# Kernel tuning notes

Hardware: AMD Instinct MI355X
Metric: run time of the kernel (lower is better)

## Reference

```python
import jax, jax.numpy as jnp
import numpy as np

N, E, F_DIM = 30000, 480000, 256
CLS_HID, NUM_CLASS, GEN_HID, MI_HID, BATCH = 128, 16, 64, 128, 4096
COM_L1, COM_L2, LAM, ALPHA, TAU, EPS = 0.5, 0.5, 0.5, 1.0, 0.5, 1e-8


def _glorot(key, shape):
    scale = jnp.sqrt(2.0 / (shape[0] + shape[-1]))
    return scale * jax.random.normal(key, shape, dtype=jnp.float32)


def setup_inputs() -> dict:
    key = jax.random.key(0)
    ks = jax.random.split(key, 32)
    inp = {
        'feat': jax.random.normal(ks[0], (N, F_DIM), dtype=jnp.float32),
        'view1_indices': jax.random.randint(ks[1], (2, E), 0, N),
        'view1_values': jax.random.uniform(ks[2], (E,), dtype=jnp.float32),
        'view2_indices': jax.random.randint(ks[3], (2, E), 0, N),
        'view2_values': jax.random.uniform(ks[4], (E,), dtype=jnp.float32),
        'idx': jnp.sort(jax.random.randint(ks[5], (BATCH,), 0, N)),
        # GenView (v1 and v2): gen_gcn weight + gen_mlp (Linear(2*gen_hid, 1))
        'W_gen_v1': _glorot(ks[6], (F_DIM, GEN_HID)),
        'Wm_v1': _glorot(ks[7], (2 * GEN_HID, 1)),
        'bm_v1': jnp.zeros((1,), dtype=jnp.float32),
        'W_gen_v2': _glorot(ks[8], (F_DIM, GEN_HID)),
        'Wm_v2': _glorot(ks[9], (2 * GEN_HID, 1)),
        'bm_v2': jnp.zeros((1,), dtype=jnp.float32),
        # Classification: three two-layer GCN encoders (v1, v2, v)
        'W1_v1': _glorot(ks[10], (F_DIM, CLS_HID)), 'W2_v1': _glorot(ks[11], (CLS_HID, NUM_CLASS)),
        'W1_v2': _glorot(ks[12], (F_DIM, CLS_HID)), 'W2_v2': _glorot(ks[13], (CLS_HID, NUM_CLASS)),
        'W1_v': _glorot(ks[14], (F_DIM, CLS_HID)), 'W2_v': _glorot(ks[15], (CLS_HID, NUM_CLASS)),
        # MI_NCE: three single GCN layers + shared projection MLP
        'Wg': _glorot(ks[16], (F_DIM, MI_HID)),
        'Wg1': _glorot(ks[17], (F_DIM, MI_HID)),
        'Wg2': _glorot(ks[18], (F_DIM, MI_HID)),
        'Wp1': _glorot(ks[19], (MI_HID, MI_HID)), 'bp1': jnp.zeros((MI_HID,), dtype=jnp.float32),
        'Wp2': _glorot(ks[20], (MI_HID, MI_HID)), 'bp2': jnp.zeros((MI_HID,), dtype=jnp.float32),
    }
    return inp


def spmm(idx, vals, x, n):
    # sparse COO adj (idx [2,E], vals [E]) @ dense x [n,d]
    return jax.ops.segment_sum(vals[:, None] * x[idx[1]], idx[0], num_segments=n)


def gcn_layer(x, idx, vals, W, n, act):
    h = spmm(idx, vals, x @ W, n)
    return jax.nn.relu(h) if act else h


def two_layer(x, idx, vals, W1, W2, n):
    return gcn_layer(gcn_layer(x, idx, vals, W1, n, True), idx, vals, W2, n, False)


def sparse_row_softmax(scores, rows, n):
    m = jax.lax.stop_gradient(jax.ops.segment_max(scores, rows, num_segments=n))
    e = jnp.exp(scores - m[rows])
    s = jax.ops.segment_sum(e, rows, num_segments=n)
    return e / s[rows]


def gen_view(feat, idx, vals, Wg, Wm, bm, com_lambda, n):
    emb = gcn_layer(feat, idx, vals, Wg, n, True)
    ff = jnp.concatenate([emb[idx[0]], emb[idx[1]]], axis=-1)  # [E, 2*gen_hid]
    temp = (ff @ Wm + bm).reshape(-1)
    pi = sparse_row_softmax(temp, idx[0], n)  # torch.sparse.softmax(dim=1)
    return vals + com_lambda * pi  # same sparsity pattern as v_ori


def sym(idx, vals):
    # normalize1 (big=True): adj + adj.T as COO concat (duplicates sum in spmm)
    return jnp.concatenate([idx, idx[::-1]], axis=1), jnp.concatenate([vals, vals])


def get_weight(prob):
    top2 = jax.lax.top_k(prob, 2)[0]
    fir, sec = top2[:, 0], top2[:, 1]
    return jnp.exp(ALPHA * (LAM * jnp.log(fir + EPS) + (1.0 - LAM) * jnp.log(fir - sec + EPS)))


def contrast_cal(z1, z2):
    num = z1 @ z2.T
    den = jnp.linalg.norm(z1, axis=-1, keepdims=True) @ jnp.linalg.norm(z2, axis=-1, keepdims=True).T
    m12 = jnp.exp(num / den / TAU)
    m21 = m12.T
    l12 = -jnp.log(jnp.diag(m12 / (m12.sum(1, keepdims=True) + EPS)) + EPS).mean()
    l21 = -jnp.log(jnp.diag(m21 / (m21.sum(1, keepdims=True) + EPS)) + EPS).mean()
    return 0.5 * (l12 + l21)


def cogsl_forward(feat, view1_values, view2_values,
                  W_gen_v1, Wm_v1, bm_v1, W_gen_v2, Wm_v2, bm_v2,
                  W1_v1, W2_v1, W1_v2, W2_v2, W1_v, W2_v,
                  Wg, Wg1, Wg2, Wp1, bp1, Wp2, bp2,
                  view1_indices, view2_indices, idx):
    n = feat.shape[0]
    # View_Estimator (GenView + normalize1)
    nv1 = gen_view(feat, view1_indices, view1_values, W_gen_v1, Wm_v1, bm_v1, COM_L1, n)
    nv2 = gen_view(feat, view2_indices, view2_values, W_gen_v2, Wm_v2, bm_v2, COM_L2, n)
    i1, v1 = sym(view1_indices, nv1)
    i2, v2 = sym(view2_indices, nv2)
    # Classification on each generated view
    prob_v1 = jax.nn.softmax(two_layer(feat, i1, v1, W1_v1, W2_v1, n), axis=1)
    prob_v2 = jax.nn.softmax(two_layer(feat, i2, v2, W1_v2, W2_v2, n), axis=1)
    logits_v1 = jnp.log(prob_v1 + EPS)
    logits_v2 = jnp.log(prob_v2 + EPS)
    # Fusion: per-node convex combination of the two sparse views (row scaling)
    w1 = get_weight(prob_v1)
    w2 = get_weight(prob_v2)
    b1 = w1 / (w1 + w2)
    b2 = w2 / (w1 + w2)
    idx_f = jnp.concatenate([i1, i2], axis=1)
    vals_f = jnp.concatenate([b1[i1[0]] * v1, b2[i2[0]] * v2])
    prob_v = jax.nn.softmax(two_layer(feat, idx_f, vals_f, W1_v, W2_v, n), axis=1)
    logits_v = jnp.log(prob_v + EPS)
    # MI_NCE over [fused v, v1, v2], big=True -> sample `batch` nodes
    proj = lambda h: jax.nn.elu(h @ Wp1 + bp1) @ Wp2 + bp2
    ev = proj(gcn_layer(feat, idx_f, vals_f, Wg, n, True))[idx]
    e1 = proj(gcn_layer(feat, i1, v1, Wg1, n, True))[idx]
    e2 = proj(gcn_layer(feat, i2, v2, Wg2, n, True))[idx]
    vv1 = contrast_cal(ev, e1)
    vv2 = contrast_cal(ev, e2)
    v1v2 = contrast_cal(e1, e2)
    return jnp.concatenate([logits_v.ravel(), logits_v1.ravel(), logits_v2.ravel(),
                            jnp.stack([vv1, vv2, v1v2])])


def reference(feat, view1_indices, view1_values, view2_indices, view2_values, idx,
              W_gen_v1, Wm_v1, bm_v1, W_gen_v2, Wm_v2, bm_v2,
              W1_v1, W2_v1, W1_v2, W2_v2, W1_v, W2_v,
              Wg, Wg1, Wg2, Wp1, bp1, Wp2, bp2):
    return cogsl_forward(feat, view1_values, view2_values,
                         W_gen_v1, Wm_v1, bm_v1, W_gen_v2, Wm_v2, bm_v2,
                         W1_v1, W2_v1, W1_v2, W2_v2, W1_v, W2_v,
                         Wg, Wg1, Wg2, Wp1, bp1, Wp2, bp2,
                         view1_indices, view2_indices, idx)
```

## Files before the change

### kernel.cpp

```cpp
#include <hip/hip_runtime.h>
#include <math.h>

#define NN 30000
#define EE 480000
#define FD 256
#define CH 128
#define NCLS 16
#define GH 64
#define MH 128
#define BT 4096
#define EPSc 1e-8f
#define GBc ((NN + 127) / 128)
#define SPB8 ((NN + 7) / 8)
#define SPB16 ((NN + 15) / 16)
#define RBc ((BT + 15) / 16)
#define PRB ((NN + 63) / 64)
#define PJB (BT / 8)
#define PX4 1056

typedef __attribute__((ext_vector_type(8))) short short8;
typedef __attribute__((ext_vector_type(4))) float f32x4;

__device__ __forceinline__ unsigned short f2bf(float x) {
    unsigned b = __float_as_uint(x);
    unsigned r = b + 0x7FFFu + ((b >> 16) & 1u);
    return (unsigned short)(r >> 16);
}
__device__ __forceinline__ float bf2f(unsigned short h) {
    return __uint_as_float(((unsigned)h) << 16);
}
__device__ __forceinline__ float4 fma4(float s, float4 x, float4 a) {
    a.x = fmaf(s, x.x, a.x); a.y = fmaf(s, x.y, a.y);
    a.z = fmaf(s, x.z, a.z); a.w = fmaf(s, x.w, a.w);
    return a;
}

struct WSArgs {
    const float* s[8];
    unsigned short* h[8];
    unsigned short* l[8];
};

__global__ __launch_bounds__(256) void prep_all(
    const float* __restrict__ feat, unsigned short* __restrict__ fhi,
    unsigned short* __restrict__ flo, WSArgs a,
    const int* __restrict__ i1, const int* __restrict__ i2, int* __restrict__ cnt,
    int* __restrict__ sd1, int* __restrict__ sd2,
    int* __restrict__ sc1, int* __restrict__ sc2)
{
    int b = blockIdx.x;
    if (b < 30000) {
        long i = (long)b * 256 + threadIdx.x;
        float v = feat[i];
        unsigned short h = f2bf(v);
        fhi[i] = h;
        flo[i] = f2bf(v - bf2f(h));
        return;
    }
    b -= 30000;
    if (b < 896) {
        int i = b * 256 + threadIdx.x;
        if (i >= 229376) return;
        constexpr int NNp[8] = {64, 64, 128, 128, 128, 128, 128, 128};
        constexpr int OFF[9] = {0, 16384, 32768, 65536, 98304, 131072, 163840, 196608, 229376};
        int w = 0;
#pragma unroll
        for (int t = 1; t < 8; t++) if (i >= OFF[t]) w = t;
        int j = i - OFF[w];
        int N = NNp[w];
        int k = j / N, n = j % N;
        float v = a.s[w][j];
        unsigned short hh = f2bf(v);
        a.h[w][(size_t)n * 256 + k] = hh;
        a.l[w][(size_t)n * 256 + k] = f2bf(v - bf2f(hh));
        return;
    }
    b -= 896;
    int e = b * 256 + threadIdx.x;
    if (e >= EE) return;
    int r1 = i1[e], c1 = i1[EE + e];
    int r2 = i2[e], c2 = i2[EE + e];
    sd1[e] = atomicAdd(&cnt[r1], 1);
    sd2[e] = atomicAdd(&cnt[NN + r2], 1);
    sc1[e] = atomicAdd(&cnt[2 * NN + c1], 1);
    sc2[e] = atomicAdd(&cnt[3 * NN + c2], 1);
}

template <int NT, bool OUT16>
__device__ __forceinline__ void gemm3_body(
    unsigned short* sm, int bx,
    const unsigned short* __restrict__ Ahi, const unsigned short* __restrict__ Alo,
    const unsigned short* __restrict__ BThi, const unsigned short* __restrict__ BTlo,
    int K, void* __restrict__ Cv, int Cstride, int M)
{
    unsigned short* Ah = sm;
    unsigned short* Al = Ah + 128 * 40;
    unsigned short* Bh = Al + 128 * 40;
    unsigned short* Bl = Bh + NT * 16 * 40;
    int t = threadIdx.x;
    int w = t >> 6, l = t & 63;
    int lane = l & 15, quad = l >> 4;
// ... 65 lines not shown
            for (int n = 0; n < NT; n++) {
                if (OUT16)
                    ((unsigned short*)Cv)[(size_t)gr * Cstride + n * 16 + lane] = f2bf(acc[s][n][reg]);
                else
                    ((float*)Cv)[(size_t)gr * Cstride + n * 16 + lane] = acc[s][n][reg];
            }
        }
    }
}

template <int NT, bool OUT16>
__device__ __forceinline__ void gemm1_body(
    unsigned short* sm, int bx,
    const unsigned short* __restrict__ Ahi,
    const unsigned short* __restrict__ BThi,
    int K, void* __restrict__ Cv, int Cstride, int M)
{
    unsigned short* Ah = sm;
    unsigned short* Bh = Ah + 128 * 40;
    int t = threadIdx.x;
    int w = t >> 6, l = t & 63;
    int lane = l & 15, quad = l >> 4;
    int row0 = bx * 128;
    f32x4 acc[2][NT];
#pragma unroll
    for (int s = 0; s < 2; s++)
#pragma unroll
        for (int n = 0; n < NT; n++) acc[s][n] = (f32x4)(0.f);

    int ar = t >> 1, ako = (t & 1) << 4;
    int nkc = K >> 5;
    for (int kc = 0; kc < nkc; kc++) {
        int kb = kc << 5;
        {
            int gr = row0 + ar;
            float4 h0, h1;
            if (gr < M) {
                const float4* pH = (const float4*)&Ahi[(size_t)gr * K + kb + ako];
                h0 = pH[0]; h1 = pH[1];
            } else {
                h0 = h1 = make_float4(0.f, 0.f, 0.f, 0.f);
            }
            float4* dH = (float4*)&Ah[ar * 40 + ako];
            dH[0] = h0; dH[1] = h1;
        }
        if (ar < NT * 16) {
            const float4* pH = (const float4*)&BThi[(size_t)ar * K + kb + ako];
            float4 h0 = pH[0], h1 = pH[1];
            float4* dH = (float4*)&Bh[ar * 40 + ako];
            dH[0] = h0; dH[1] = h1;
        }
        __syncthreads();
        short8 aH[2];
#pragma unroll
        for (int s = 0; s < 2; s++)
            aH[s] = *(const short8*)&Ah[(w * 32 + s * 16 + lane) * 40 + quad * 8];
#pragma unroll
        for (int n = 0; n < NT; n++) {
            short8 bH = *(const short8*)&Bh[(n * 16 + lane) * 40 + quad * 8];
#pragma unroll
            for (int s = 0; s < 2; s++)
                acc[s][n] = __builtin_amdgcn_mfma_f32_16x16x32_bf16(aH[s], bH, acc[s][n], 0, 0, 0);
        }
        __syncthreads();
    }
#pragma unroll
    for (int s = 0; s < 2; s++) {
        int rb = row0 + w * 32 + s * 16 + quad * 4;
#pragma unroll
        for (int reg = 0; reg < 4; reg++) {
            int gr = rb + reg;
            if (gr >= M) continue;
#pragma unroll
            for (int n = 0; n < NT; n++) {
                if (OUT16)
                    ((unsigned short*)Cv)[(size_t)gr * Cstride + n * 16 + lane] = f2bf(acc[s][n][reg]);
                else
                    ((float*)Cv)[(size_t)gr * Cstride + n * 16 + lane] = acc[s][n][reg];
            }
        }
    }
}

__global__ __launch_bounds__(256) void mega1x(
    const int* __restrict__ i1, const float* __restrict__ v1,
    const int* __restrict__ i2, const float* __restrict__ v2,
    const int* __restrict__ sd1, const int* __restrict__ sd2,
    const int* __restrict__ sc1, const int* __restrict__ sc2,
    const int* __restrict__ rp4,
    int2* __restrict__ ed1, int2* __restrict__ ec1,
    int2* __restrict__ ed2, int2* __restrict__ ec2,
    const unsigned short* __restrict__ feat_hi, const unsigned short* __restrict__ feat_lo,
    const unsigned short* __restrict__ wgen12h, const unsigned short* __restrict__ wgen12l,
    float* __restrict__ Pg,
    const unsigned short* __restrict__ w1pairh, const unsigned short* __restrict__ w1pairl,
    float* __restrict__ P01,
    const unsigned short* __restrict__ w1vh, unsigned short* __restrict__ Ph2,
    const unsigned short* __restrict__ wgallh, unsigned short* __restrict__ Pmi16)
{
    __shared__ unsigned short sm[128 * 40 * 2 + 8 * 16 * 40 * 2];
    int b = blockIdx.x;
    if (b < GBc) {
        gemm3_body<8, false>(sm, b, feat_hi, feat_lo, wgen12h, wgen12l, FD, Pg, 128, NN);
        return;
    }
    b -= GBc;
    if (b < 2 * GBc) {
        int y = b / GBc, bx = b % GBc;
        gemm3_body<8, false>(sm, bx, feat_hi, feat_lo,
                             w1pairh + (size_t)y * 32768, w1pairl + (size_t)y * 32768,
                             FD, P01 + (size_t)y * 128, 256, NN);
        return;
    }
    b -= 2 * GBc;
    if (b < GBc) {
        gemm1_body<8, true>(sm, b, feat_hi, w1vh, FD, Ph2, 128, NN);
        return;
    }
    b -= GBc;
    if (b < 3 * GBc) {
        int y = b / GBc, bx = b % GBc;
        gemm1_body<8, true>(sm, bx, feat_hi, wgallh + (size_t)y * 32768,
                            FD, Pmi16 + (size_t)y * 128, 384, NN);
        return;
    }
    b -= 3 * GBc;
    int e = b * 256 + threadIdx.x;
    if (e >= EE) return;
    const int* rp_d1 = rp4;
    const int* rp_d2 = rp4 + (NN + 1);
    const int* rp_c1 = rp4 + 2 * (NN + 1);
    const int* rp_c2 = rp4 + 3 * (NN + 1);
    int r = i1[e], c = i1[EE + e];
    int p = rp_d1[r] + sd1[e];
    ed1[p] = make_int2(c, __float_as_int(v1[e]));
    ec1[rp_c1[c] + sc1[e]] = make_int2(r, p);
    r = i2[e]; c = i2[EE + e];
    p = rp_d2[r] + sd2[e];
    ed2[p] = make_int2(c, __float_as_int(v2[e]));
    ec2[rp_c2[c] + sc2[e]] = make_int2(r, p);
}

__global__ __launch_bounds__(256) void contrast_direct(
    const unsigned short* __restrict__ z16, float* __restrict__ stats)
{
    int p = blockIdx.z;
    int pa = (p == 2) ? 1 : 0;
    int pb = (p == 0) ? 1 : 2;
    const unsigned short* A = z16 + (size_t)pa * BT * MH;
    const unsigned short* B = z16 + (size_t)pb * BT * MH;
    float* diag = stats + (size_t)p * 3 * BT;
    float* rs = diag + BT;
    float* cs = rs + BT;
    int t = threadIdx.x;
    int w = t >> 6, l = t & 63, m = l & 15, quad = l >> 4;
    int i0 = blockIdx.y * 128, j0 = blockIdx.x * 128;

    short8 afr[2][4];
#pragma unroll
    for (int s = 0; s < 2; s++) {
        const unsigned short* arow = &A[(size_t)(i0 + w * 32 + s * 16 + m) * MH + quad * 8];
#pragma unroll
        for (int kc = 0; kc < 4; kc++)
            afr[s][kc] = *(const short8*)(arow + kc * 32);
    }
    f32x4 acc[2][8];
#pragma unroll
    for (int s = 0; s < 2; s++)
#pragma unroll
        for (int n = 0; n < 8; n++) acc[s][n] = (f32x4)(0.f);

#pragma unroll
    for (int kc = 0; kc < 4; kc++) {
#pragma unroll
        for (int n = 0; n < 8; n++) {
            short8 bf = *(const short8*)&B[(size_t)(j0 + n * 16 + m) * MH + kc * 32 + quad * 8];
            acc[0][n] = __builtin_amdgcn_mfma_f32_16x16x32_bf16(afr[0][kc], bf, acc[0][n], 0, 0, 0);
            acc[1][n] = __builtin_amdgcn_mfma_f32_16x16x32_bf16(afr[1][kc], bf, acc[1][n], 0, 0, 0);
        }
    }
    float colp[8];
#pragma unroll
    for (int n = 0; n < 8; n++) colp[n] = 0.f;
#pragma unroll
    for (int s = 0; s < 2; s++) {
        int rbase = i0 + w * 32 + s * 16 + quad * 4;
#pragma unroll
        for (int reg = 0; reg < 4; reg++) {
            float rsum = 0.f;
            int gi = rbase + reg;
#pragma unroll
            for (int n = 0; n < 8; n++) {
                float mv = expf(acc[s][n][reg] * 2.0f);
                rsum += mv;
                colp[n] += mv;
                int gj = j0 + n * 16 + m;
                if (gi == gj) diag[gi] = mv;
            }
            rsum += __shfl_xor(rsum, 1); rsum += __shfl_xor(rsum, 2);
            rsum += __shfl_xor(rsum, 4); rsum += __shfl_xor(rsum, 8);
            if (m == 0) atomicAdd(&rs[gi], rsum);
        }
    }
    __shared__ float scol[128];
    if (t < 128) scol[t] = 0.f;
    __syncthreads();
#pragma unroll
    for (int n = 0; n < 8; n++) {
        float v = colp[n];
        v += __shfl_xor(v, 16); v += __shfl_xor(v, 32);
        if (quad == (n & 3)) atomicAdd(&scol[n * 16 + m], v);
    }
    __syncthreads();
    if (t < 128) atomicAdd(&cs[j0 + t], scol[t]);
}

__global__ __launch_bounds__(1024) void scan_block4(const int* __restrict__ cnt,
                                                    int* __restrict__ rowptr,
                                                    int* __restrict__ bsum) {
    int y = blockIdx.y;
    int* rp = rowptr + y * (NN + 1);
    int* bs = bsum + y * 32;
    __shared__ int tmp[1024];
    int t = threadIdx.x;
    int i = blockIdx.x * 1024 + t;
    int v = (i < NN) ? cnt[y * NN + i] : 0;
    tmp[t] = v;
    __syncthreads();
    for (int off = 1; off < 1024; off <<= 1) {
        int add = (t >= off) ? tmp[t - off] : 0;
        __syncthreads();
        tmp[t] += add;
        __syncthreads();
    }
    if (i <= NN) rp[i] = tmp[t] - v;
    if (t == 1023) bs[blockIdx.x] = tmp[1023];
}
__global__ void scan_bsum4(int* __restrict__ bsum, int nb) {
    bsum += blockIdx.x * 32;
    int t = threadIdx.x;
    int orig = (t < nb) ? bsum[t] : 0;
    int v = orig;
    for (int off = 1; off < 64; off <<= 1) {
        int u = __shfl_up(v, off);
        if (t >= off) v += u;
    }
    if (t < nb) bsum[t] = v - orig;
}
__global__ void scan_add4(const int* __restrict__ bsum, int* __restrict__ rowptr) {
    int y = blockIdx.y;
    const int* bs = bsum + y * 32;
    int* rp = rowptr + y * (NN + 1);
    int i = blockIdx.x * 1024 + threadIdx.x;
    if (i <= NN) rp[i] += bs[blockIdx.x];
}

__global__ __launch_bounds__(256) void gen_nv(
    const int* __restrict__ rp_d, int2* __restrict__ ed1, int2* __restrict__ ed2,
    const float* __restrict__ sb, float* __restrict__ nvd1, float* __restrict__ nvd2)
{
    int y = blockIdx.y;
    int row = blockIdx.x * 256 + threadIdx.x;
    if (row >= NN) return;
    const int* rp = rp_d + y * (NN + 1);
    int2* ed = y ? ed2 : ed1;
    float* nvd = y ? nvd2 : nvd1;
    const float* sbv = sb + (size_t)y * NN;
    int p0 = rp[row], p1 = rp[row + 1];
    float m = -3.4e38f, sum = 0.f;
    for (int j = p0; j < p1; j++) {
        float x = sbv[ed[j].x];
        if (x > m) { sum = sum * expf(m - x) + 1.f; m = x; }
        else sum += expf(x - m);
    }
    float inv = 1.f / sum;
    for (int j = p0; j < p1; j++) {
        int2 q = ed[j];
        float nv = __int_as_float(q.y) + 0.5f * expf(sbv[q.x] - m) * inv;
        nvd[j] = nv;
        ed[j].y = __float_as_int(nv);
    }
}

template <int STR4>
__device__ __forceinline__ void gath_dir_f32(
    const int* __restrict__ rp, const int2* __restrict__ ed, int row,
    const float4* __restrict__ x4, int xo, float4* a)
{
    int p0 = rp[row], p1 = rp[row + 1];
    int j = p0;
    for (; j + 8 <= p1; j += 8) {
        int2 q0 = ed[j], q1 = ed[j+1], q2 = ed[j+2], q3 = ed[j+3];
        int2 q4 = ed[j+4], q5 = ed[j+5], q6 = ed[j+6], q7 = ed[j+7];
        float4 x0 = x4[(size_t)q0.x * STR4 + xo];
        float4 x1 = x4[(size_t)q1.x * STR4 + xo];
        float4 x2 = x4[(size_t)q2.x * STR4 + xo];
        float4 x3 = x4[(size_t)q3.x * STR4 + xo];
        float4 x5 = x4[(size_t)q4.x * STR4 + xo];
        float4 x6 = x4[(size_t)q5.x * STR4 + xo];
        float4 x7 = x4[(size_t)q6.x * STR4 + xo];
        float4 x8 = x4[(size_t)q7.x * STR4 + xo];
        a[0] = fma4(__int_as_float(q0.y), x0, a[0]);
        a[1] = fma4(__int_as_float(q1.y), x1, a[1]);
        a[2] = fma4(__int_as_float(q2.y), x2, a[2]);
        a[3] = fma4(__int_as_float(q3.y), x3, a[3]);
        a[0] = fma4(__int_as_float(q4.y), x5, a[0]);
        a[1] = fma4(__int_as_float(q5.y), x6, a[1]);
        a[2] = fma4(__int_as_float(q6.y), x7, a[2]);
        a[3] = fma4(__int_as_float(q7.y), x8, a[3]);
    }
    for (; j + 4 <= p1; j += 4) {
        int2 q0 = ed[j], q1 = ed[j+1], q2 = ed[j+2], q3 = ed[j+3];
        a[0] = fma4(__int_as_float(q0.y), x4[(size_t)q0.x * STR4 + xo], a[0]);
        a[1] = fma4(__int_as_float(q1.y), x4[(size_t)q1.x * STR4 + xo], a[1]);
        a[2] = fma4(__int_as_float(q2.y), x4[(size_t)q2.x * STR4 + xo], a[2]);
        a[3] = fma4(__int_as_float(q3.y), x4[(size_t)q3.x * STR4 + xo], a[3]);
    }
    for (; j < p1; j++) {
        int2 q = ed[j];
        a[0] = fma4(__int_as_float(q.y), x4[(size_t)q.x * STR4 + xo], a[0]);
    }
}
template <int STR4>
__device__ __forceinline__ void gath_csc_f32(
    const int* __restrict__ rp, const int2* __restrict__ ec, const float* __restrict__ nvd,
    int row, const float4* __restrict__ x4, int xo, float4* a)
{
    int p0 = rp[row], p1 = rp[row + 1];
    int j = p0;
    for (; j + 8 <= p1; j += 8) {
        int2 q0 = ec[j], q1 = ec[j+1], q2 = ec[j+2], q3 = ec[j+3];
        int2 q4 = ec[j+4], q5 = ec[j+5], q6 = ec[j+6], q7 = ec[j+7];
        float4 x0 = x4[(size_t)q0.x * STR4 + xo];
        float4 x1 = x4[(size_t)q1.x * STR4 + xo];
        float4 x2 = x4[(size_t)q2.x * STR4 + xo];
        float4 x3 = x4[(size_t)q3.x * STR4 + xo];
        float4 x5 = x4[(size_t)q4.x * STR4 + xo];
        float4 x6 = x4[(size_t)q5.x * STR4 + xo];
        float4 x7 = x4[(size_t)q6.x * STR4 + xo];
        float4 x8 = x4[(size_t)q7.x * STR4 + xo];
        float v0 = nvd[q0.y], v1 = nvd[q1.y], v2 = nvd[q2.y], v3 = nvd[q3.y];
        float v4 = nvd[q4.y], v5 = nvd[q5.y], v6 = nvd[q6.y], v7 = nvd[q7.y];
        a[0] = fma4(v0, x0, a[0]);
        a[1] = fma4(v1, x1, a[1]);
        a[2] = fma4(v2, x2, a[2]);
        a[3] = fma4(v3, x3, a[3]);
        a[0] = fma4(v4, x5, a[0]);
        a[1] = fma4(v5, x6, a[1]);
        a[2] = fma4(v6, x7, a[2]);
        a[3] = fma4(v7, x8, a[3]);
    }
    for (; j + 4 <= p1; j += 4) {
        int2 q0 = ec[j], q1 = ec[j+1], q2 = ec[j+2], q3 = ec[j+3];
        float v0 = nvd[q0.y], v1 = nvd[q1.y], v2 = nvd[q2.y], v3 = nvd[q3.y];
        a[0] = fma4(v0, x4[(size_t)q0.x * STR4 + xo], a[0]);
        a[1] = fma4(v1, x4[(size_t)q1.x * STR4 + xo], a[1]);
        a[2] = fma4(v2, x4[(size_t)q2.x * STR4 + xo], a[2]);
        a[3] = fma4(v3, x4[(size_t)q3.x * STR4 + xo], a[3]);
    }
    for (; j < p1; j++) {
        int2 q = ec[j];
        a[0] = fma4(nvd[q.y], x4[(size_t)q.x * STR4 + xo], a[0]);
    }
}

__global__ __launch_bounds__(256) void spmm64_scores(
    const int* __restrict__ rp_d, const int2* __restrict__ e1, const int2* __restrict__ e2,
    const float* __restrict__ Pg, const float* __restrict__ Wm1,
    const float* __restrict__ Wm2, float* __restrict__ sb)
{
    int y = blockIdx.y;
    const int* rp = rp_d + y * (NN + 1);
    const int2* arr = y ? e2 : e1;
    int row = blockIdx.x * 16 + threadIdx.x / 16;
    int o = threadIdx.x % 16;
    if (row >= NN) return;
    float4 a[4] = {};
    gath_dir_f32<32>(rp, arr, row, (const float4*)Pg, y * 16 + o, a);
    float4 r;
    r.x = fmaxf((a[0].x + a[1].x) + (a[2].x + a[3].x), 0.f);
    r.y = fmaxf((a[0].y + a[1].y) + (a[2].y + a[3].y), 0.f);
    r.z = fmaxf((a[0].z + a[1].z) + (a[2].z + a[3].z), 0.f);
    r.w = fmaxf((a[0].w + a[1].w) + (a[2].w + a[3].w), 0.f);
    const float* Wmh = (y ? Wm2 : Wm1) + GH;
    float part = r.x * Wmh[o * 4] + r.y * Wmh[o * 4 + 1]
               + r.z * Wmh[o * 4 + 2] + r.w * Wmh[o * 4 + 3];
    part += __shfl_xor(part, 1); part += __shfl_xor(part, 2);
    part += __shfl_xor(part, 4); part += __shfl_xor(part, 8);
    if (o == 0) sb[y * NN + row] = part;
}

__device__ __forceinline__ void softmax16_epi(
    float4 r, int node, float* __restrict__ logits, float* __restrict__ wout)
{
    int o = threadIdx.x & 3;
    float mx = fmaxf(fmaxf(r.x, r.y), fmaxf(r.z, r.w));
    mx = fmaxf(mx, __shfl_xor(mx, 1));
    mx = fmaxf(mx, __shfl_xor(mx, 2));
    float e0 = expf(r.x - mx), e1 = expf(r.y - mx), e2 = expf(r.z - mx), e3 = expf(r.w - mx);
    float s = (e0 + e1) + (e2 + e3);
    s += __shfl_xor(s, 1);
    s += __shfl_xor(s, 2);
    float inv = 1.f / s;
    float p0 = e0 * inv, p1 = e1 * inv, p2 = e2 * inv, p3 = e3 * inv;
    float4 lg;
    lg.x = logf(p0 + EPSc); lg.y = logf(p1 + EPSc);
    lg.z = logf(p2 + EPSc); lg.w = logf(p3 + EPSc);
    ((float4*)logits)[(size_t)node * 4 + o] = lg;
    if (wout) {
        float f = p0, se = -1.f;
        if (p1 > f) { se = f; f = p1; } else se = p1;
        if (p2 > f) { se = f; f = p2; } else if (p2 > se) se = p2;
        if (p3 > f) { se = f; f = p3; } else if (p3 > se) se = p3;
#pragma unroll
        for (int d = 1; d <= 2; d <<= 1) {
            float of = __shfl_xor(f, d), os = __shfl_xor(se, d);
            if (of > f) { se = fmaxf(f, os); f = of; }
            else se = fmaxf(se, of);
        }
        if (o == 0)
            wout[node] = expf(0.5f * logf(f + EPSc) + 0.5f * logf(f - se + EPSc));
    }
}

__device__ __forceinline__ void pair_body(
    int y, int bx, const int* __restrict__ rp_d, const int* __restrict__ rp_c,
    const int2* __restrict__ ed1, const int2* __restrict__ ec1, const float* __restrict__ nvd1,
    const int2* __restrict__ ed2, const int2* __restrict__ ec2, const float* __restrict__ nvd2,
    const float* __restrict__ R01, float* __restrict__ logits_base, float* __restrict__ w12)
{
    const int* rpd = rp_d + y * (NN + 1);
    const int* rpc = rp_c + y * (NN + 1);
    const int2* ed = y ? ed2 : ed1;
    const int2* ec = y ? ec2 : ec1;
    const float* nvd = y ? nvd2 : nvd1;
    int row = bx * 64 + threadIdx.x / 4;
    int o = threadIdx.x % 4;
    if (row >= NN) return;
    const float4* x4 = (const float4*)(R01 + (size_t)y * NN * 16);
    float4 a[4] = {};
    gath_dir_f32<4>(rpd, ed, row, x4, o, a);
    gath_csc_f32<4>(rpc, ec, nvd, row, x4, o, a);
    float4 r;
    r.x = (a[0].x + a[1].x) + (a[2].x + a[3].x);
    r.y = (a[0].y + a[1].y) + (a[2].y + a[3].y);
    r.z = (a[0].z + a[1].z) + (a[2].z + a[3].z);
    r.w = (a[0].w + a[1].w) + (a[2].w + a[3].w);
    softmax16_epi(r, row, logits_base + (size_t)y * NN * NCLS, w12 + (size_t)y * NN);
}

__device__ __forceinline__ void fused_body(
    int bx, const int* __restrict__ rp_d, const int* __restrict__ rp_c,
    const int2* __restrict__ ed1, const int2* __restrict__ ec1, const float* __restrict__ nvd1,
    const int2* __restrict__ ed2, const int2* __restrict__ ec2, const float* __restrict__ nvd2,
    const float* __restrict__ w12, const float* __restrict__ x, float* __restrict__ logits)
{
    int row = bx * 64 + threadIdx.x / 4;
    int o = threadIdx.x % 4;
    if (row >= NN) return;
    const float4* x4 = (const float4*)x;
    float4 a[4] = {};
    gath_dir_f32<4>(rp_d, ed1, row, x4, o, a);
    gath_csc_f32<4>(rp_c, ec1, nvd1, row, x4, o, a);
    float4 s1;
    s1.x = (a[0].x + a[1].x) + (a[2].x + a[3].x);
    s1.y = (a[0].y + a[1].y) + (a[2].y + a[3].y);
    s1.z = (a[0].z + a[1].z) + (a[2].z + a[3].z);
    s1.w = (a[0].w + a[1].w) + (a[2].w + a[3].w);
    float4 b[4] = {};
    gath_dir_f32<4>(rp_d + (NN + 1), ed2, row, x4, o, b);
    gath_csc_f32<4>(rp_c + (NN + 1), ec2, nvd2, row, x4, o, b);
    float4 s2;
// ... 220 lines not shown

__global__ __launch_bounds__(256) void mega2(
    const int* __restrict__ rp_d, const int* __restrict__ rp_c,
    const int2* __restrict__ ed1, const int2* __restrict__ ec1, const float* __restrict__ nvd1,
    const int2* __restrict__ ed2, const int2* __restrict__ ec2, const float* __restrict__ nvd2,
    const float* __restrict__ P01, const float* __restrict__ W2v1, const float* __restrict__ W2v2,
    float* __restrict__ R01,
    const int* __restrict__ rows, const unsigned short* __restrict__ Pmi,
    float* __restrict__ zQ)
{
    __shared__ float sm[2048 + 8 * 128];
    int b = blockIdx.x;
    if (b < 2 * SPB8) {
        int y = b / SPB8;
        spmm128f_body(sm, b % SPB8, y, rp_d, rp_c, y ? ed2 : ed1, y ? ec2 : ec1,
                      y ? nvd2 : nvd1, P01, y ? W2v2 : W2v1, R01);
        return;
    }
    b -= 2 * SPB8;
    int y = 1 + b / RBc;
    rows_b16_body(b % RBc, y, rp_d, rp_c, ed1, ec1, nvd1, ed2, ec2, nvd2,
                  rows, Pmi, zQ);
}

__device__ __forceinline__ void proj8_body(
    float* g, float* u, float* red, int bx, int plane,
    const float* __restrict__ zQ,
    const float* __restrict__ Wp1, const float* __restrict__ bp1,
    const float* __restrict__ Wp2, const float* __restrict__ bp2,
    unsigned short* __restrict__ z16)
{
    int t = threadIdx.x;
    size_t base = (size_t)plane * BT + (size_t)bx * 8;
    for (int idx = t; idx < 8 * MH; idx += 256)
        g[idx] = zQ[(base + (idx >> 7)) * MH + (idx & 127)];
    __syncthreads();
    int col = t & 127;
    int rh = t >> 7;
    float acc[4];
    float b1 = bp1[col];
#pragma unroll
    for (int rr = 0; rr < 4; rr++) acc[rr] = b1;
    for (int k = 0; k < MH; k++) {
        float wk = Wp1[k * MH + col];
#pragma unroll
        for (int rr = 0; rr < 4; rr++)
            acc[rr] = fmaf(g[(rh * 4 + rr) * MH + k], wk, acc[rr]);
    }
#pragma unroll
    for (int rr = 0; rr < 4; rr++)
        u[(rh * 4 + rr) * MH + col] = acc[rr] > 0.f ? acc[rr] : (expf(acc[rr]) - 1.f);
    __syncthreads();
    float z[4];
    float b2 = bp2[col];
#pragma unroll
    for (int rr = 0; rr < 4; rr++) z[rr] = b2;
    for (int k = 0; k < MH; k++) {
        float wk = Wp2[k * MH + col];
#pragma unroll
        for (int rr = 0; rr < 4; rr++)
            z[rr] = fmaf(u[(rh * 4 + rr) * MH + k], wk, z[rr]);
    }
    float sq[4];
#pragma unroll
    for (int rr = 0; rr < 4; rr++) sq[rr] = z[rr] * z[rr];
#pragma unroll
    for (int off = 32; off; off >>= 1) {
#pragma unroll
        for (int rr = 0; rr < 4; rr++) sq[rr] += __shfl_xor(sq[rr], off);
    }
    int w = t >> 6;
    if ((t & 63) == 0) {
#pragma unroll
        for (int rr = 0; rr < 4; rr++) red[w * 4 + rr] = sq[rr];
    }
    __syncthreads();
#pragma unroll
    for (int rr = 0; rr < 4; rr++) {
        float nrm = sqrtf(red[(rh * 2) * 4 + rr] + red[(rh * 2 + 1) * 4 + rr]);
        z16[(base + rh * 4 + rr) * MH + col] = f2bf(z[rr] / nrm);
    }
}

__global__ __launch_bounds__(256) void pairX(
    const int* __restrict__ rp_d, const int* __restrict__ rp_c,
    const int2* __restrict__ ed1, const int2* __restrict__ ec1, const float* __restrict__ nvd1,
    const int2* __restrict__ ed2, const int2* __restrict__ ec2, const float* __restrict__ nvd2,
    const float* __restrict__ R01, float* __restrict__ logits_base, float* __restrict__ w12,
    const unsigned short* __restrict__ Ph2, float* __restrict__ A1, float* __restrict__ A2,
    const int* __restrict__ rows, const unsigned short* __restrict__ Pmi,
    float* __restrict__ G1, float* __restrict__ G2,
    const float* __restrict__ zQ,
    const float* __restrict__ Wp1, const float* __restrict__ bp1,
    const float* __restrict__ Wp2, const float* __restrict__ bp2,
    unsigned short* __restrict__ z16)
{
    __shared__ float psm[2064];
    int b = blockIdx.x;
    int u = b >> 2, r = b & 3;
    if (r == 0) {
        if (u < 2 * PRB)
            pair_body(u / PRB, u % PRB, rp_d, rp_c, ed1, ec1, nvd1, ed2, ec2, nvd2,
                      R01, logits_base, w12);
        return;
    }
    int idx = u * 3 + (r - 1);
    if (idx < SPB16) {
        b2gather_body(idx, rp_d, rp_c, ed1, ec1, nvd1, ed2, ec2, nvd2, Ph2, A1, A2);
        return;
    }
    idx -= SPB16;
    if (idx < RBc) {
        rows0_gather_body(idx, rp_d, rp_c, ed1, ec1, nvd1, ed2, ec2, nvd2,
                          rows, Pmi, G1, G2);
        return;
    }
    idx -= RBc;
    if (idx < 2 * PJB) {
        int plane = 1 + idx / PJB;
        proj8_body(psm, psm + 1024, psm + 2048, idx % PJB, plane,
                   zQ, Wp1, bp1, Wp2, bp2, z16);
    }
}

__global__ __launch_bounds__(256) void combineB2(
    const float* __restrict__ w12,
    const float* __restrict__ A1, const float* __restrict__ A2,
    const float* __restrict__ W2v, float* __restrict__ R2,
    const int* __restrict__ rows,
    const float* __restrict__ G1, const float* __restrict__ G2,
    float* __restrict__ zQ)
{
    __shared__ float sm[2048 + 16 * 128];
    int b = blockIdx.x;
    int r = threadIdx.x / 16;
    int o = threadIdx.x % 16;
    if (b < SPB16) {
        float* W2s = sm;
        float* Qs  = sm + 2048;
        for (int i = threadIdx.x; i < 2048; i += 256) W2s[i] = W2v[i];
        int row = b * 16 + r;
        float wa = w12[row], wb = w12[NN + row];
        float inv = 1.f / (wa + wb);
        float w1 = wa * inv, w2 = wb * inv;
        const float* p1 = A1 + (size_t)row * 128 + o * 8;
        const float* p2 = A2 + (size_t)row * 128 + o * 8;
#pragma unroll
        for (int k = 0; k < 8; k++)
            Qs[r * 128 + o * 8 + k] = fmaxf(w1 * p1[k] + w2 * p2[k], 0.f);
        __syncthreads();
        int t = threadIdx.x;
        int rr = t >> 4, c = t & 15;
        int grow = b * 16 + rr;
        float acc = 0.f;
        const float* qrow = &Qs[rr * 128];
#pragma unroll 8
        for (int k = 0; k < 128; k++)
            acc = fmaf(qrow[k], W2s[k * 16 + c], acc);
        R2[(size_t)grow * 16 + c] = acc;
        return;
    }
    b -= SPB16;
    int ri = b * 16 + r;
    if (ri >= BT) return;
    int node = rows[ri];
    float wa = w12[node], wb = w12[NN + node];
    float inv = 1.f / (wa + wb);
    float w1 = wa * inv, w2 = wb * inv;
    const float* p1 = G1 + (size_t)ri * 128 + o * 8;
    const float* p2 = G2 + (size_t)ri * 128 + o * 8;
    float* out = zQ + (size_t)ri * 128 + o * 8;
#pragma unroll
    for (int k = 0; k < 8; k++)
        out[k] = fmaxf(w1 * p1[k] + w2 * p2[k], 0.f);
}

__global__ __launch_bounds__(256) void fusedX(
    const int* __restrict__ rp_d, const int* __restrict__ rp_c,
    const int2* __restrict__ ed1, const int2* __restrict__ ec1, const float* __restrict__ nvd1,
    const int2* __restrict__ ed2, const int2* __restrict__ ec2, const float* __restrict__ nvd2,
    const float* __restrict__ w12, const float* __restrict__ R2, float* __restrict__ logits,
    const float* __restrict__ zQ,
    const float* __restrict__ Wp1, const float* __restrict__ bp1,
    const float* __restrict__ Wp2, const float* __restrict__ bp2,
    unsigned short* __restrict__ z16)
{
    __shared__ float psm[2064];
    int b = blockIdx.x;
    if (b < PRB) {
        fused_body(b, rp_d, rp_c, ed1, ec1, nvd1, ed2, ec2, nvd2, w12, R2, logits);
        return;
    }
    proj8_body(psm, psm + 1024, psm + 2048, b - PRB, 0, zQ, Wp1, bp1, Wp2, bp2, z16);
}

__global__ void contrast_reduce(const float* __restrict__ stats, float* __restrict__ out3)
{
    int p = blockIdx.x, t = threadIdx.x;
    const float* diag = stats + (size_t)p * 3 * BT;
    const float* rs = diag + BT;
    const float* cs = rs + BT;
    float s1 = 0.f, s2 = 0.f;
    for (int i = t; i < BT; i += 256) {
        float d = diag[i];
        s1 += logf(d / (rs[i] + EPSc) + EPSc);
        s2 += logf(d / (cs[i] + EPSc) + EPSc);
    }
#pragma unroll
    for (int off = 32; off; off >>= 1) { s1 += __shfl_down(s1, off); s2 += __shfl_down(s2, off); }
    __shared__ float sh[8];
    if ((t & 63) == 0) { sh[(t >> 6) * 2] = s1; sh[(t >> 6) * 2 + 1] = s2; }
    __syncthreads();
    if (t == 0) {
        float a = sh[0] + sh[2] + sh[4] + sh[6];
        float b = sh[1] + sh[3] + sh[5] + sh[7];
        out3[p] = 0.5f * (-a / BT - b / BT);
    }
}

extern "C" void kernel_launch(void* const* d_in, const int* in_sizes, int n_in,
                              void* d_out, int out_size, void* d_ws, size_t ws_size,
                              hipStream_t stream)
{
    const float* feat   = (const float*)d_in[0];
    const int*   ind1   = (const int*)d_in[1];
    const float* vals1  = (const float*)d_in[2];
    const int*   ind2   = (const int*)d_in[3];
    const float* vals2  = (const float*)d_in[4];
    const int*   idxb   = (const int*)d_in[5];
    const float* Wm1    = (const float*)d_in[7];
    const float* Wm2    = (const float*)d_in[10];
    const float* W2_v1  = (const float*)d_in[13];
    const float* W2_v2  = (const float*)d_in[15];
    const float* W2_v   = (const float*)d_in[17];
    const float* Wp1    = (const float*)d_in[21];
    const float* bp1    = (const float*)d_in[22];
    const float* Wp2    = (const float*)d_in[23];
    const float* bp2    = (const float*)d_in[24];
    float* dout = (float*)d_out;

    float* ws = (float*)d_ws;
    size_t off = 0;
    auto alloc = [&](size_t n) { n = (n + 3) & ~(size_t)3; float* p = ws + off; off += n; return p; };
    auto alloc_s = [&](size_t n) { return (unsigned short*)alloc((n + 1) / 2); };

    float* pool = alloc(16000000);
    float* Pg   = pool;
    float* P01  = pool + 3840000;
    float* R01  = pool + 11520000;
    float* zQ   = pool + 12480000;
    float* A1   = pool;
    float* G1   = pool + 14052864;
    float* G2   = pool + 14577152;
    float* R2   = pool + 15101440;

    unsigned short* feat_hi = alloc_s((size_t)NN * FD);
    unsigned short* feat_lo = alloc_s((size_t)NN * FD);
    float* A2 = (float*)feat_hi;
    unsigned short* Ph2d    = alloc_s((size_t)NN * CH);
    unsigned short* Pmi16d  = alloc_s((size_t)NN * 384);
    float* sb   = alloc(2 * NN);
    float* w12  = alloc(2 * NN);
    float* stats = alloc((size_t)3 * 3 * BT);
    unsigned short* z16 = alloc_s((size_t)3 * BT * MH);
    int2* ed1 = (int2*)alloc(2 * (size_t)EE);
    int2* ed2 = (int2*)alloc(2 * (size_t)EE);
    int2* ec1 = (int2*)alloc(2 * (size_t)EE);
    int2* ec2 = (int2*)alloc(2 * (size_t)EE);
    float* nvd1 = alloc(EE);
    float* nvd2 = alloc(EE);
    int* sd1 = (int*)alloc(EE);
    int* sd2 = (int*)alloc(EE);
    int* sc1 = (int*)alloc(EE);
    int* sc2 = (int*)alloc(EE);
    int* rp4  = (int*)alloc(4 * (NN + 1));
    int* cnt4 = (int*)alloc(4 * NN);
    int* bsum = (int*)alloc(128);
    int* rp_d = rp4;
    int* rp_c = rp4 + 2 * (NN + 1);
    unsigned short* wgen12h = alloc_s(32768); unsigned short* wgen12l = alloc_s(32768);
    unsigned short* w1pairh = alloc_s(65536); unsigned short* w1pairl = alloc_s(65536);
    unsigned short* w1vh    = alloc_s(32768); unsigned short* w1vl    = alloc_s(32768);
    unsigned short* wgallh  = alloc_s(98304); unsigned short* wgalll  = alloc_s(98304);

    const int NB = (NN + 1 + 1023) / 1024;
    const int NCNT = (EE + 255) / 256;

    hipMemsetAsync(cnt4, 0, 4 * NN * 4, stream);
    WSArgs a;
    a.s[0] = (const float*)d_in[6];  a.h[0] = wgen12h;          a.l[0] = wgen12l;
    a.s[1] = (const float*)d_in[9];  a.h[1] = wgen12h + 16384;  a.l[1] = wgen12l + 16384;
    a.s[2] = (const float*)d_in[12]; a.h[2] = w1pairh;          a.l[2] = w1pairl;
    a.s[3] = (const float*)d_in[14]; a.h[3] = w1pairh + 32768;  a.l[3] = w1pairl + 32768;
    a.s[4] = (const float*)d_in[16]; a.h[4] = w1vh;             a.l[4] = w1vl;
    a.s[5] = (const float*)d_in[18]; a.h[5] = wgallh;           a.l[5] = wgalll;
    a.s[6] = (const float*)d_in[19]; a.h[6] = wgallh + 32768;   a.l[6] = wgalll + 32768;
    a.s[7] = (const float*)d_in[20]; a.h[7] = wgallh + 65536;   a.l[7] = wgalll + 65536;
    prep_all<<<30000 + 896 + NCNT, 256, 0, stream>>>(feat, feat_hi, feat_lo, a,
                                                     ind1, ind2, cnt4, sd1, sd2, sc1, sc2);

    scan_block4<<<dim3(NB, 4), 1024, 0, stream>>>(cnt4, rp4, bsum);
    scan_bsum4<<<4, 64, 0, stream>>>(bsum, NB);
    scan_add4<<<dim3(NB, 4), 1024, 0, stream>>>(bsum, rp4);

    mega1x<<<7 * GBc + NCNT, 256, 0, stream>>>(ind1, vals1, ind2, vals2,
                                               sd1, sd2, sc1, sc2, rp4,
                                               ed1, ec1, ed2, ec2,
                                               feat_hi, feat_lo, wgen12h, wgen12l, Pg,
                                               w1pairh, w1pairl, P01,
                                               w1vh, Ph2d, wgallh, Pmi16d);

    spmm64_scores<<<dim3((NN + 15) / 16, 2), 256, 0, stream>>>(rp_d, ed1, ed2, Pg, Wm1, Wm2, sb);
    gen_nv<<<dim3((NN + 255) / 256, 2), 256, 0, stream>>>(rp_d, ed1, ed2, sb, nvd1, nvd2);
    hipMemsetAsync(stats, 0, (size_t)3 * 3 * BT * 4, stream);

    mega2<<<2 * SPB8 + 2 * RBc, 256, 0, stream>>>(rp_d, rp_c, ed1, ec1, nvd1,
                                                  ed2, ec2, nvd2, P01, W2_v1, W2_v2,
                                                  R01, idxb, Pmi16d, zQ);

    pairX<<<4 * PX4, 256, 0, stream>>>(rp_d, rp_c, ed1, ec1, nvd1, ed2, ec2, nvd2,
                                       R01, dout + (size_t)NN * NCLS, w12,
                                       Ph2d, A1, A2, idxb, Pmi16d, G1, G2,
                                       zQ, Wp1, bp1, Wp2, bp2, z16);

    combineB2<<<SPB16 + RBc, 256, 0, stream>>>(w12, A1, A2, W2_v, R2, idxb, G1, G2, zQ);

    fusedX<<<PRB + PJB, 256, 0, stream>>>(rp_d, rp_c, ed1, ec1, nvd1, ed2, ec2, nvd2,
                                          w12, R2, dout, zQ, Wp1, bp1, Wp2, bp2, z16);

    contrast_direct<<<dim3(32, 32, 3), 256, 0, stream>>>(z16, stats);
    contrast_reduce<<<3, 256, 0, stream>>>(stats, dout + (size_t)3 * NN * NCLS);
}
```

Baseline: 746.1 us.

## Overlap dense GEMMs with score SpMM and move one contrast pair earlier

The remaining feature GEMMs (P01, Ph2, Pmi16) move out of the edge-scatter megakernel into a new kernel that interleaves them 1:3 with the gen-view score SpMM blocks. This lets memory-bound gather work overlap with MFMA work. The v1-v2 contrast pair (p=2), which only needs z16 rows already produced by pairX, now runs as extra blocks of combineB2, so the final contrast launch covers two pairs instead of three. gen_nv also batches its edge loads eight at a time to raise memory-level parallelism. The risks are heavier block-dispatch logic and shared-memory reuse in combineB2.

Result: slower. 840.7 us (+12.7%).

```diff
diff --git a/kernel.cpp b/kernel.cpp
--- a/kernel.cpp
+++ b/kernel.cpp
@@ -17,6 +17,8 @@
 #define PRB ((NN + 63) / 64)
 #define PJB (BT / 8)
 #define PX4 1056
+#define SXB 1410
+#define S64B ((NN + 15) / 16)
 
 typedef __attribute__((ext_vector_type(8))) short short8;
 typedef __attribute__((ext_vector_type(4))) float f32x4;
@@ -248,7 +250,7 @@
     }
 }
 
-__global__ __launch_bounds__(256) void mega1x(
+__global__ __launch_bounds__(256) void mega1a(
     const int* __restrict__ i1, const float* __restrict__ v1,
     const int* __restrict__ i2, const float* __restrict__ v2,
     const int* __restrict__ sd1, const int* __restrict__ sd2,
@@ -258,11 +260,7 @@
     int2* __restrict__ ed2, int2* __restrict__ ec2,
     const unsigned short* __restrict__ feat_hi, const unsigned short* __restrict__ feat_lo,
     const unsigned short* __restrict__ wgen12h, const unsigned short* __restrict__ wgen12l,
-    float* __restrict__ Pg,
-    const unsigned short* __restrict__ w1pairh, const unsigned short* __restrict__ w1pairl,
-    float* __restrict__ P01,
-    const unsigned short* __restrict__ w1vh, unsigned short* __restrict__ Ph2,
-    const unsigned short* __restrict__ wgallh, unsigned short* __restrict__ Pmi16)
+    float* __restrict__ Pg)
 {
     __shared__ unsigned short sm[128 * 40 * 2 + 8 * 16 * 40 * 2];
     int b = blockIdx.x;
@@ -271,26 +269,6 @@
         return;
     }
     b -= GBc;
-    if (b < 2 * GBc) {
-        int y = b / GBc, bx = b % GBc;
-        gemm3_body<8, false>(sm, bx, feat_hi, feat_lo,
-                             w1pairh + (size_t)y * 32768, w1pairl + (size_t)y * 32768,
-                             FD, P01 + (size_t)y * 128, 256, NN);
-        return;
-    }
-    b -= 2 * GBc;
-    if (b < GBc) {
-        gemm1_body<8, true>(sm, b, feat_hi, w1vh, FD, Ph2, 128, NN);
-        return;
-    }
-    b -= GBc;
-    if (b < 3 * GBc) {
-        int y = b / GBc, bx = b % GBc;
-        gemm1_body<8, true>(sm, bx, feat_hi, wgallh + (size_t)y * 32768,
-                            FD, Pmi16 + (size_t)y * 128, 384, NN);
-        return;
-    }
-    b -= 3 * GBc;
     int e = b * 256 + threadIdx.x;
     if (e >= EE) return;
     const int* rp_d1 = rp4;
@@ -305,80 +283,6 @@
     p = rp_d2[r] + sd2[e];
     ed2[p] = make_int2(c, __float_as_int(v2[e]));
     ec2[rp_c2[c] + sc2[e]] = make_int2(r, p);
-}
-
-__global__ __launch_bounds__(256) void contrast_direct(
-    const unsigned short* __restrict__ z16, float* __restrict__ stats)
-{
-    int p = blockIdx.z;
-    int pa = (p == 2) ? 1 : 0;
-    int pb = (p == 0) ? 1 : 2;
-    const unsigned short* A = z16 + (size_t)pa * BT * MH;
-    const unsigned short* B = z16 + (size_t)pb * BT * MH;
-    float* diag = stats + (size_t)p * 3 * BT;
-    float* rs = diag + BT;
-    float* cs = rs + BT;
-    int t = threadIdx.x;
-    int w = t >> 6, l = t & 63, m = l & 15, quad = l >> 4;
-    int i0 = blockIdx.y * 128, j0 = blockIdx.x * 128;
-
-    short8 afr[2][4];
-#pragma unroll
-    for (int s = 0; s < 2; s++) {
-        const unsigned short* arow = &A[(size_t)(i0 + w * 32 + s * 16 + m) * MH + quad * 8];
-#pragma unroll
-        for (int kc = 0; kc < 4; kc++)
-            afr[s][kc] = *(const short8*)(arow + kc * 32);
-    }
-    f32x4 acc[2][8];
-#pragma unroll
-    for (int s = 0; s < 2; s++)
-#pragma unroll
-        for (int n = 0; n < 8; n++) acc[s][n] = (f32x4)(0.f);
-
-#pragma unroll
-    for (int kc = 0; kc < 4; kc++) {
-#pragma unroll
-        for (int n = 0; n < 8; n++) {
-            short8 bf = *(const short8*)&B[(size_t)(j0 + n * 16 + m) * MH + kc * 32 + quad * 8];
-            acc[0][n] = __builtin_amdgcn_mfma_f32_16x16x32_bf16(afr[0][kc], bf, acc[0][n], 0, 0, 0);
-            acc[1][n] = __builtin_amdgcn_mfma_f32_16x16x32_bf16(afr[1][kc], bf, acc[1][n], 0, 0, 0);
-        }
-    }
-    float colp[8];
-#pragma unroll
-    for (int n = 0; n < 8; n++) colp[n] = 0.f;
-#pragma unroll
-    for (int s = 0; s < 2; s++) {
-        int rbase = i0 + w * 32 + s * 16 + quad * 4;
-#pragma unroll
-        for (int reg = 0; reg < 4; reg++) {
-            float rsum = 0.f;
-            int gi = rbase + reg;
-#pragma unroll
-            for (int n = 0; n < 8; n++) {
-                float mv = expf(acc[s][n][reg] * 2.0f);
-                rsum += mv;
-                colp[n] += mv;
-                int gj = j0 + n * 16 + m;
-                if (gi == gj) diag[gi] = mv;
-            }
-            rsum += __shfl_xor(rsum, 1); rsum += __shfl_xor(rsum, 2);
-            rsum += __shfl_xor(rsum, 4); rsum += __shfl_xor(rsum, 8);
-            if (m == 0) atomicAdd(&rs[gi], rsum);
-        }
-    }
-    __shared__ float scol[128];
-    if (t < 128) scol[t] = 0.f;
-    __syncthreads();
-#pragma unroll
-    for (int n = 0; n < 8; n++) {
-        float v = colp[n];
-        v += __shfl_xor(v, 16); v += __shfl_xor(v, 32);
-        if (quad == (n & 3)) atomicAdd(&scol[n * 16 + m], v);
-    }
-    __syncthreads();
-    if (t < 128) atomicAdd(&cs[j0 + t], scol[t]);
 }
 
 __global__ __launch_bounds__(1024) void scan_block4(const int* __restrict__ cnt,
@@ -434,17 +338,39 @@
     const float* sbv = sb + (size_t)y * NN;
     int p0 = rp[row], p1 = rp[row + 1];
     float m = -3.4e38f, sum = 0.f;
-    for (int j = p0; j < p1; j++) {
-        float x = sbv[ed[j].x];
-        if (x > m) { sum = sum * expf(m - x) + 1.f; m = x; }
-        else sum += expf(x - m);
+    for (int j = p0; j < p1; j += 8) {
+        int cnt = p1 - j; if (cnt > 8) cnt = 8;
+        float x[8];
+#pragma unroll
+        for (int e = 0; e < 8; e++)
+            x[e] = (e < cnt) ? sbv[ed[j + e].x] : 0.f;
+#pragma unroll
+        for (int e = 0; e < 8; e++) {
+            if (e < cnt) {
+                float xx = x[e];
+                if (xx > m) { sum = sum * expf(m - xx) + 1.f; m = xx; }
+                else sum += expf(xx - m);
+            }
+        }
     }
     float inv = 1.f / sum;
-    for (int j = p0; j < p1; j++) {
-        int2 q = ed[j];
-        float nv = __int_as_float(q.y) + 0.5f * expf(sbv[q.x] - m) * inv;
-        nvd[j] = nv;
-        ed[j].y = __float_as_int(nv);
+    for (int j = p0; j < p1; j += 8) {
+        int cnt = p1 - j; if (cnt > 8) cnt = 8;
+        int2 q[8]; float x[8];
+#pragma unroll
+        for (int e = 0; e < 8; e++)
+            q[e] = (e < cnt) ? ed[j + e] : make_int2(0, 0);
+#pragma unroll
+        for (int e = 0; e < 8; e++)
+            x[e] = (e < cnt) ? sbv[q[e].x] : 0.f;
+#pragma unroll
+        for (int e = 0; e < 8; e++) {
+            if (e < cnt) {
+                float nv = __int_as_float(q[e].y) + 0.5f * expf(x[e] - m) * inv;
+                nvd[j + e] = nv;
+                ed[j + e].y = __float_as_int(nv);
+            }
+        }
     }
 }
 
@@ -530,15 +456,15 @@
     }
 }
 
-__global__ __launch_bounds__(256) void spmm64_scores(
-    const int* __restrict__ rp_d, const int2* __restrict__ e1, const int2* __restrict__ e2,
+__device__ __forceinline__ void spmm64_body(
+    int y, int bx, const int* __restrict__ rp_d,
+    const int2* __restrict__ e1, const int2* __restrict__ e2,
     const float* __restrict__ Pg, const float* __restrict__ Wm1,
     const float* __restrict__ Wm2, float* __restrict__ sb)
 {
-    int y = blockIdx.y;
     const int* rp = rp_d + y * (NN + 1);
     const int2* arr = y ? e2 : e1;
-    int row = blockIdx.x * 16 + threadIdx.x / 16;
+    int row = bx * 16 + threadIdx.x / 16;
     int o = threadIdx.x % 16;
     if (row >= NN) return;
     float4 a[4] = {};
@@ -554,6 +480,45 @@
     part += __shfl_xor(part, 1); part += __shfl_xor(part, 2);
     part += __shfl_xor(part, 4); part += __shfl_xor(part, 8);
     if (o == 0) sb[y * NN + row] = part;
+}
+
+__global__ __launch_bounds__(256) void spmmX(
+    const int* __restrict__ rp_d, const int2* __restrict__ ed1, const int2* __restrict__ ed2,
+    const float* __restrict__ Pg, const float* __restrict__ Wm1,
+    const float* __restrict__ Wm2, float* __restrict__ sb,
+    const unsigned short* __restrict__ feat_hi, const unsigned short* __restrict__ feat_lo,
+    const unsigned short* __restrict__ w1pairh, const unsigned short* __restrict__ w1pairl,
+    float* __restrict__ P01,
+    const unsigned short* __restrict__ w1vh, unsigned short* __restrict__ Ph2,
+    const unsigned short* __restrict__ wgallh, unsigned short* __restrict__ Pmi16)
+{
+    __shared__ unsigned short sm[128 * 40 * 2 + 8 * 16 * 40 * 2];
+    int b = blockIdx.x;
+    int u = b >> 2, r = b & 3;
+    if (r == 3) {
+        if (u < 2 * GBc) {
+            int y = u / GBc, bx = u % GBc;
+            gemm3_body<8, false>(sm, bx, feat_hi, feat_lo,
+                                 w1pairh + (size_t)y * 32768, w1pairl + (size_t)y * 32768,
+                                 FD, P01 + (size_t)y * 128, 256, NN);
+            return;
+        }
+        u -= 2 * GBc;
+        if (u < GBc) {
+            gemm1_body<8, true>(sm, u, feat_hi, w1vh, FD, Ph2, 128, NN);
+            return;
+        }
+        u -= GBc;
+        if (u < 3 * GBc) {
+            int y = u / GBc, bx = u % GBc;
+            gemm1_body<8, true>(sm, bx, feat_hi, wgallh + (size_t)y * 32768,
+                                FD, Pmi16 + (size_t)y * 128, 384, NN);
+        }
+        return;
+    }
+    int s = u * 3 + r;
+    if (s >= 2 * S64B) return;
+    spmm64_body(s / S64B, s % S64B, rp_d, ed1, ed2, Pg, Wm1, Wm2, sb);
 }
 
 __device__ __forceinline__ void softmax16_epi(
@@ -940,6 +905,85 @@
     }
 }
 
+__device__ __forceinline__ void contrast_body(
+    int p, int i0, int j0,
+    const unsigned short* __restrict__ z16, float* __restrict__ stats, float* scol)
+{
+    int pa = (p == 2) ? 1 : 0;
+    int pb = (p == 0) ? 1 : 2;
+    const unsigned short* A = z16 + (size_t)pa * BT * MH;
+    const unsigned short* B = z16 + (size_t)pb * BT * MH;
+    float* diag = stats + (size_t)p * 3 * BT;
+    float* rs = diag + BT;
+    float* cs = rs + BT;
+    int t = threadIdx.x;
+    int w = t >> 6, l = t & 63, m = l & 15, quad = l >> 4;
+
+    short8 afr[2][4];
+#pragma unroll
+    for (int s = 0; s < 2; s++) {
+        const unsigned short* arow = &A[(size_t)(i0 + w * 32 + s * 16 + m) * MH + quad * 8];
+#pragma unroll
+        for (int kc = 0; kc < 4; kc++)
+            afr[s][kc] = *(const short8*)(arow + kc * 32);
+    }
+    f32x4 acc[2][8];
+#pragma unroll
+    for (int s = 0; s < 2; s++)
+#pragma unroll
+        for (int n = 0; n < 8; n++) acc[s][n] = (f32x4)(0.f);
+
+#pragma unroll
+    for (int kc = 0; kc < 4; kc++) {
+#pragma unroll
+        for (int n = 0; n < 8; n++) {
+            short8 bf = *(const short8*)&B[(size_t)(j0 + n * 16 + m) * MH + kc * 32 + quad * 8];
+            acc[0][n] = __builtin_amdgcn_mfma_f32_16x16x32_bf16(afr[0][kc], bf, acc[0][n], 0, 0, 0);
+            acc[1][n] = __builtin_amdgcn_mfma_f32_16x16x32_bf16(afr[1][kc], bf, acc[1][n], 0, 0, 0);
+        }
+    }
+    float colp[8];
+#pragma unroll
+    for (int n = 0; n < 8; n++) colp[n] = 0.f;
+#pragma unroll
+    for (int s = 0; s < 2; s++) {
+        int rbase = i0 + w * 32 + s * 16 + quad * 4;
+#pragma unroll
+        for (int reg = 0; reg < 4; reg++) {
+            float rsum = 0.f;
+            int gi = rbase + reg;
+#pragma unroll
+            for (int n = 0; n < 8; n++) {
+                float mv = expf(acc[s][n][reg] * 2.0f);
+                rsum += mv;
+                colp[n] += mv;
+                int gj = j0 + n * 16 + m;
+                if (gi == gj) diag[gi] = mv;
+            }
+            rsum += __shfl_xor(rsum, 1); rsum += __shfl_xor(rsum, 2);
+            rsum += __shfl_xor(rsum, 4); rsum += __shfl_xor(rsum, 8);
+            if (m == 0) atomicAdd(&rs[gi], rsum);
+        }
+    }
+    if (t < 128) scol[t] = 0.f;
+    __syncthreads();
+#pragma unroll
+    for (int n = 0; n < 8; n++) {
+        float v = colp[n];
+        v += __shfl_xor(v, 16); v += __shfl_xor(v, 32);
+        if (quad == (n & 3)) atomicAdd(&scol[n * 16 + m], v);
+    }
+    __syncthreads();
+    if (t < 128) atomicAdd(&cs[j0 + t], scol[t]);
+}
+
+__global__ __launch_bounds__(256) void contrast_direct(
+    const unsigned short* __restrict__ z16, float* __restrict__ stats)
+{
+    __shared__ float scol[128];
+    contrast_body(blockIdx.z, blockIdx.y * 128, blockIdx.x * 128, z16, stats, scol);
+}
+
 __global__ __launch_bounds__(256) void pairX(
     const int* __restrict__ rp_d, const int* __restrict__ rp_c,
     const int2* __restrict__ ed1, const int2* __restrict__ ec1, const float* __restrict__ nvd1,
@@ -987,7 +1031,8 @@
     const float* __restrict__ W2v, float* __restrict__ R2,
     const int* __restrict__ rows,
     const float* __restrict__ G1, const float* __restrict__ G2,
-    float* __restrict__ zQ)
+    float* __restrict__ zQ,
+    const unsigned short* __restrict__ z16, float* __restrict__ stats)
 {
     __shared__ float sm[2048 + 16 * 128];
     int b = blockIdx.x;
@@ -1011,26 +1056,31 @@
         int rr = t >> 4, c = t & 15;
         int grow = b * 16 + rr;
         float acc = 0.f;
-        const float* qrow = &Qs[rr * 128];
+        const float* qrow = &sm[2048 + rr * 128];
 #pragma unroll 8
         for (int k = 0; k < 128; k++)
-            acc = fmaf(qrow[k], W2s[k * 16 + c], acc);
+            acc = fmaf(qrow[k], sm[k * 16 + c], acc);
         R2[(size_t)grow * 16 + c] = acc;
         return;
     }
     b -= SPB16;
-    int ri = b * 16 + r;
-    if (ri >= BT) return;
-    int node = rows[ri];
-    float wa = w12[node], wb = w12[NN + node];
-    float inv = 1.f / (wa + wb);
-    float w1 = wa * inv, w2 = wb * inv;
-    const float* p1 = G1 + (size_t)ri * 128 + o * 8;
-    const float* p2 = G2 + (size_t)ri * 128 + o * 8;
-    float* out = zQ + (size_t)ri * 128 + o * 8;
-#pragma unroll
-    for (int k = 0; k < 8; k++)
-        out[k] = fmaxf(w1 * p1[k] + w2 * p2[k], 0.f);
+    if (b < RBc) {
+        int ri = b * 16 + r;
+        if (ri >= BT) return;
+        int node = rows[ri];
+        float wa = w12[node], wb = w12[NN + node];
+        float inv = 1.f / (wa + wb);
+        float w1 = wa * inv, w2 = wb * inv;
+        const float* p1 = G1 + (size_t)ri * 128 + o * 8;
+        const float* p2 = G2 + (size_t)ri * 128 + o * 8;
+        float* out = zQ + (size_t)ri * 128 + o * 8;
+#pragma unroll
+        for (int k = 0; k < 8; k++)
+            out[k] = fmaxf(w1 * p1[k] + w2 * p2[k], 0.f);
+        return;
+    }
+    b -= RBc;
+    contrast_body(2, (b >> 5) * 128, (b & 31) * 128, z16, stats, sm);
 }
 
 __global__ __launch_bounds__(256) void fusedX(
@@ -1161,14 +1211,15 @@
     scan_bsum4<<<4, 64, 0, stream>>>(bsum, NB);
     scan_add4<<<dim3(NB, 4), 1024, 0, stream>>>(bsum, rp4);
 
-    mega1x<<<7 * GBc + NCNT, 256, 0, stream>>>(ind1, vals1, ind2, vals2,
-                                               sd1, sd2, sc1, sc2, rp4,
-                                               ed1, ec1, ed2, ec2,
-                                               feat_hi, feat_lo, wgen12h, wgen12l, Pg,
-                                               w1pairh, w1pairl, P01,
-                                               w1vh, Ph2d, wgallh, Pmi16d);
-
-    spmm64_scores<<<dim3((NN + 15) / 16, 2), 256, 0, stream>>>(rp_d, ed1, ed2, Pg, Wm1, Wm2, sb);
+    mega1a<<<GBc + NCNT, 256, 0, stream>>>(ind1, vals1, ind2, vals2,
+                                           sd1, sd2, sc1, sc2, rp4,
+                                           ed1, ec1, ed2, ec2,
+                                           feat_hi, feat_lo, wgen12h, wgen12l, Pg);
+
+    spmmX<<<4 * SXB, 256, 0, stream>>>(rp_d, ed1, ed2, Pg, Wm1, Wm2, sb,
+                                       feat_hi, feat_lo, w1pairh, w1pairl, P01,
+                                       w1vh, Ph2d, wgallh, Pmi16d);
+
     gen_nv<<<dim3((NN + 255) / 256, 2), 256, 0, stream>>>(rp_d, ed1, ed2, sb, nvd1, nvd2);
     hipMemsetAsync(stats, 0, (size_t)3 * 3 * BT * 4, stream);
 
@@ -1181,11 +1232,12 @@
                                        Ph2d, A1, A2, idxb, Pmi16d, G1, G2,
                                        zQ, Wp1, bp1, Wp2, bp2, z16);
 
-    combineB2<<<SPB16 + RBc, 256, 0, stream>>>(w12, A1, A2, W2_v, R2, idxb, G1, G2, zQ);
+    combineB2<<<SPB16 + RBc + 1024, 256, 0, stream>>>(w12, A1, A2, W2_v, R2, idxb,
+                                                      G1, G2, zQ, z16, stats);
 
     fusedX<<<PRB + PJB, 256, 0, stream>>>(rp_d, rp_c, ed1, ec1, nvd1, ed2, ec2, nvd2,
                                           w12, R2, dout, zQ, Wp1, bp1, Wp2, bp2, z16);
 
-    contrast_direct<<<dim3(32, 32, 3), 256, 0, stream>>>(z16, stats);
+    contrast_direct<<<dim3(32, 32, 2), 256, 0, stream>>>(z16, stats);
     contrast_reduce<<<3, 256, 0, stream>>>(stats, dout + (size_t)3 * NN * NCLS);
 }
```
